# Kernel optimization log

Measured on AMD Instinct MI355X. Metric: run time of the kernel, lower is better.

The kernel has to match this reference:

```python
import jax, jax.numpy as jnp
import numpy as np

DIM = 2048
NUM_HEADS = 8
HEAD_DIM = DIM // NUM_HEADS  # 256; forward requires seq_len == HEAD_DIM
B = 64
N = HEAD_DIM  # q @ k (untransposed) only works when N == head_dim


def setup_inputs() -> dict:
    key = jax.random.key(0)
    k1, k2, k3, k4 = jax.random.split(key, 4)
    x = jax.random.normal(k1, (B, N, DIM), dtype=jnp.float32)
    # torch Linear stores weight as [out_features, in_features]
    w_qkv = jax.random.normal(k2, (3 * DIM, DIM), dtype=jnp.float32) * 0.02
    w_proj = jax.random.normal(k3, (DIM, DIM), dtype=jnp.float32) * 0.02
    b_proj = jax.random.normal(k4, (DIM,), dtype=jnp.float32) * 0.02
    return {"x": x, "w_qkv": w_qkv, "w_proj": w_proj, "b_proj": b_proj}


def reference(x, w_qkv, w_proj, b_proj):
    Bb, Nn, C = x.shape
    H, D = NUM_HEADS, C // NUM_HEADS
    # qkv projection (no bias), split into q,k,v of shape [B,H,N,D]
    qkv = (x @ w_qkv.T).reshape(Bb, Nn, 3, H, D).transpose(2, 0, 3, 1, 4)
    q, k, v = qkv[0], qkv[1], qkv[2]
    # NON-standard: q @ k with k NOT transposed -> contracts q's feature dim
    # against k's token dim (valid because D == N). attn: [B,H,N,N]
    attn = jnp.matmul(q, k)
    # transpose last two dims, then softmax over the new last axis
    attn = jnp.swapaxes(attn, -2, -1)
    attn = jax.nn.softmax(attn, axis=-1)
    out = jnp.matmul(attn, v)              # [B,H,N,D]
    out = out.swapaxes(1, 2).reshape(Bb, Nn, C)
    return out @ w_proj.T + b_proj
```

## Files before the change

### kernel.cpp

```cpp
#include <hip/hip_runtime.h>
#include <hip/hip_bf16.h>

typedef unsigned short u16;
typedef __attribute__((ext_vector_type(4))) float f32x4;
typedef __attribute__((ext_vector_type(8))) short short8;
typedef __attribute__((ext_vector_type(8))) u16 us8;


__device__ __forceinline__ u16 f2bf(float f) {
  union { float f; unsigned u; } v; v.f = f;
  unsigned r = v.u + 0x7fffu + ((v.u >> 16) & 1u);
  return (u16)(r >> 16);
}
__device__ __forceinline__ float bf2f(u16 h) {
  union { unsigned u; float f; } v; v.u = ((unsigned)h) << 16; return v.f;
}

__global__ void beacon_kernel(float* __restrict__ out, float val, int n) {
  int stride = gridDim.x * blockDim.x;
  for (int i = blockIdx.x * blockDim.x + threadIdx.x; i < n; i += stride)
    out[i] = val;
}

__global__ void split_kernel(const float* __restrict__ in, u16* __restrict__ hi,
                             u16* __restrict__ lo, int n4) {
  int stride = gridDim.x * blockDim.x;
  for (int i = blockIdx.x * blockDim.x + threadIdx.x; i < n4; i += stride) {
    f32x4 v = ((const f32x4*)in)[i];
    ushort4 h;
    h.x = f2bf(v[0]); h.y = f2bf(v[1]); h.z = f2bf(v[2]); h.w = f2bf(v[3]);
    ((ushort4*)hi)[i] = h;
    if (lo) {
      ushort4 l;
      l.x = f2bf(v[0] - bf2f(h.x)); l.y = f2bf(v[1] - bf2f(h.y));
      l.z = f2bf(v[2] - bf2f(h.z)); l.w = f2bf(v[3] - bf2f(h.w));
      ((ushort4*)lo)[i] = l;
    }
  }
}

#define LGKM0 do { asm volatile("s_waitcnt lgkmcnt(0)" ::: "memory"); \
                   __builtin_amdgcn_sched_barrier(0); } while (0)
#define VMDRAIN do { asm volatile("s_waitcnt vmcnt(0)" ::: "memory"); } while (0)
#define BAR __builtin_amdgcn_s_barrier()

template<int EPI>
__global__ __launch_bounds__(512, 2)
void gemm256(const u16* __restrict__ A0, const u16* __restrict__ A1,
             const u16* __restrict__ B0, const u16* __restrict__ B1,
             int ldA, int ldB, int ntiles, int segShift, int gridMx,
             u16* __restrict__ qh, u16* __restrict__ ql,
             u16* __restrict__ kh, u16* __restrict__ kl,
             u16* __restrict__ vv,
             float* __restrict__ fout, const float* __restrict__ bias) {
  extern __shared__ __align__(16) u16 lds[];

  const int tid = threadIdx.x;
  const int w = tid >> 6, lane = tid & 63;
  const int wr = w >> 2, wcn = w & 3;
  const int l15 = lane & 15, g = lane >> 4;
  const int rsw = l15 & 7;
  const int scol = (((tid & 7) ^ ((tid >> 3) & 7)) << 3);

  int bid = blockIdx.x, cpx = gridDim.x >> 3;
  int swz = (bid & 7) * cpx + (bid >> 3);
  int m0 = (swz % gridMx) << 8;
  int n0 = (swz / gridMx) << 8;

  const u16* As[2] = {A0, A1};
  const u16* Bs[2] = {B0, B1};
  const int kmask = (1 << segShift) - 1;

  f32x4 acc[8][4] = {};
  short8 af[8], bA[4], bB[4];

  auto stageA = [&](int db, const u16* Ab, int k0) {
    #pragma unroll
    for (int s = 0; s < 4; ++s) {
      const u16* src = Ab + (size_t)(m0 + s * 64 + (tid >> 3)) * ldA + k0 + scol;
      u16* dst = lds + db * 32768 + s * 4096 + tid * 8;
      __builtin_amdgcn_global_load_lds(
          (const __attribute__((address_space(1))) unsigned*)src,
          (__attribute__((address_space(3))) unsigned*)dst, 16, 0, 0);
    }
  };
  auto stageB = [&](int db, const u16* Bb, int k0) {
    #pragma unroll
    for (int s = 0; s < 4; ++s) {
      const u16* src = Bb + (size_t)(n0 + s * 64 + (tid >> 3)) * ldB + k0 + scol;
      u16* dst = lds + db * 32768 + 16384 + s * 4096 + tid * 8;
      __builtin_amdgcn_global_load_lds(
          (const __attribute__((address_space(1))) unsigned*)src,
          (__attribute__((address_space(3))) unsigned*)dst, 16, 0, 0);
    }
  };
  auto readA = [&](int db, int MH) {
    #pragma unroll
    for (int f = 0; f < 4; ++f) {
      int row = wr * 128 + MH * 64 + f * 16 + l15;
      #pragma unroll
      for (int kk = 0; kk < 2; ++kk) {
        int sl = (kk * 4 + g) ^ rsw;
        af[f * 2 + kk] = *(const short8*)(lds + db * 32768 + row * 64 + sl * 8);
      }
    }
  };
  auto readB = [&](short8* bf, int db, int NH) {
    #pragma unroll
    for (int f = 0; f < 2; ++f) {
      int row = wcn * 64 + NH * 32 + f * 16 + l15;
      #pragma unroll
      for (int kk = 0; kk < 2; ++kk) {
        int sl = (kk * 4 + g) ^ rsw;
        bf[f * 2 + kk] = *(const short8*)(lds + db * 32768 + 16384 + row * 64 + sl * 8);
      }
    }
  };

#define MMA_QUAD(MH, NH, BF)                                                   \
  __builtin_amdgcn_s_setprio(1);                                               \
  _Pragma("unroll") for (int f = 0; f < 4; ++f)                                \
    _Pragma("unroll") for (int j = 0; j < 2; ++j)                              \
      _Pragma("unroll") for (int kk = 0; kk < 2; ++kk)                         \
        acc[(MH) * 4 + f][(NH) * 2 + j] =                                      \
            __builtin_amdgcn_mfma_f32_16x16x32_bf16(                           \
                af[f * 2 + kk], BF[j * 2 + kk],                                \
                acc[(MH) * 4 + f][(NH) * 2 + j], 0, 0, 0);                     \
  __builtin_amdgcn_s_setprio(0)

  const int T = ntiles;
  stageA(0, As[0], 0);
  stageB(0, Bs[0], 0);
  VMDRAIN;
  BAR;
  __builtin_amdgcn_sched_barrier(0);

  for (int t = 0; t < T - 1; ++t) {
    int cur = t & 1, nxt = cur ^ 1;
    int t1 = t + 1;
    const u16* An = As[t1 >> segShift];
    const u16* Bn = Bs[t1 >> segShift];
    int kn = (t1 & kmask) << 6;
    readA(cur, 0);
    readB(bA, cur, 0);
    stageA(nxt, An, kn);
    BAR; LGKM0;
    MMA_QUAD(0, 0, bA);
    BAR; __builtin_amdgcn_sched_barrier(0);
    readB(bB, cur, 1);
    stageB(nxt, Bn, kn);
    BAR; LGKM0;
    MMA_QUAD(0, 1, bB);
    BAR; __builtin_amdgcn_sched_barrier(0);
    readA(cur, 1);
    BAR; LGKM0;
    MMA_QUAD(1, 1, bB);
    BAR; __builtin_amdgcn_sched_barrier(0);
    MMA_QUAD(1, 0, bA);
    VMDRAIN;
    BAR; __builtin_amdgcn_sched_barrier(0);
  }
  {
    int cur = (T - 1) & 1;
    readA(cur, 0);
    readB(bA, cur, 0);
    LGKM0;
    MMA_QUAD(0, 0, bA);
    readB(bB, cur, 1);
    LGKM0;
    MMA_QUAD(0, 1, bB);
    readA(cur, 1);
    LGKM0;
    MMA_QUAD(1, 1, bB);
    MMA_QUAD(1, 0, bA);
  }
#undef MMA_QUAD

  #pragma unroll
  for (int i = 0; i < 8; ++i)
    #pragma unroll
    for (int j = 0; j < 4; ++j)
      #pragma unroll
      for (int rr = 0; rr < 4; ++rr) {
        int gm = m0 + wr * 128 + i * 16 + g * 4 + rr;
        int gn = n0 + wcn * 64 + j * 16 + l15;
        float val = acc[i][j][rr];
        if constexpr (EPI == 0) {
          int b = gm >> 8, tok = gm & 255;
          int sel = gn >> 11, head = (gn >> 8) & 7, col = gn & 255;
          size_t addr = (((size_t)b * 8 + head) * 256 + tok) * 256 + col;
          u16 h = f2bf(val), lo = f2bf(val - bf2f(h));
          if (sel == 0) { qh[addr] = h; ql[addr] = lo; }
          else          { kh[addr] = h; kl[addr] = lo; }
        } else if constexpr (EPI == 1) {
          int b = gm >> 8, tok = gm & 255;
          int head = (gn >> 8) & 7, col = gn & 255;
          size_t addr = (((size_t)b * 8 + head) * 256 + tok) * 256 + col;
          vv[addr] = f2bf(val);
        } else {
          fout[(size_t)gm * 2048 + gn] = val + bias[gn];
        }
      }
}

template<int EPI, int SWZ>
__global__ __launch_bounds__(256)
void gemm_nt(const u16* __restrict__ A0, const u16* __restrict__ A1, const u16* __restrict__ A2,
             const u16* __restrict__ B0, const u16* __restrict__ B1, const u16* __restrict__ B2,
             float* __restrict__ sout, u16* __restrict__ aout,
             int ksteps, int segShift, int plane_base) {
  __shared__ __align__(16) u16 lds[8192];
  u16* sA = lds;
  u16* sB = lds + 4096;

  const int tid = threadIdx.x;
  const int wave = tid >> 6, lane = tid & 63;
  const int wr = wave >> 1, wc = wave & 1;
  const int l15 = lane & 15, l16 = lane >> 4;
  const int sxor = (l15 >> 1) & 3;

  size_t zoffA = 0, zoffB = 0;
  if constexpr (EPI == 2) {
    size_t gz = (size_t)(plane_base + blockIdx.z) * 65536;
    zoffA = gz; zoffB = gz;
  }
  if constexpr (EPI == 3) {
    zoffA = (size_t)blockIdx.z * 65536;
    zoffB = (size_t)(plane_base + blockIdx.z) * 65536;
  }
  const u16* As[3] = {A0 + zoffA, A1 + zoffA, A2 + zoffA};
  const u16* Bs[3] = {B0 + zoffB, B1 + zoffB, B2 + zoffB};

  const int m0 = blockIdx.x << 7;
  const int n0 = blockIdx.y << 7;
  const int kmask = (1 << segShift) - 1;

  f32x4 acc[4][4] = {};

  auto stage = [&](const u16* gp, int ld, u16* slot, int row0, int k0) {
    int scol = ((lane & 3) ^ ((lane >> 3) & 3)) * 8;
    #pragma unroll
    for (int c = 0; c < 2; ++c) {
      int chunk = wave + c * 4;
      int r = chunk * 16 + (lane >> 2);
      const u16* src = gp + (size_t)(row0 + r) * ld + (k0 + scol);
      __builtin_amdgcn_global_load_lds(
          (const __attribute__((address_space(1))) unsigned*)src,
          (__attribute__((address_space(3))) unsigned*)(slot + chunk * 512), 16, 0, 0);
    }
  };

  for (int ks = 0; ks < ksteps; ++ks) {
    int seg = ks >> segShift;
    int k0 = (ks & kmask) * 32;
    stage(As[seg], 256, sA, m0, k0);
    stage(Bs[seg], 256, sB, n0, k0);
    __syncthreads();

    short8 a[4], b[4];
    #pragma unroll
    for (int i = 0; i < 4; ++i) {
      int ra = (wr * 64 + i * 16 + l15) * 4 + (l16 ^ sxor);
      int rb = (wc * 64 + i * 16 + l15) * 4 + (l16 ^ sxor);
      a[i] = ((const short8*)sA)[ra];
      b[i] = ((const short8*)sB)[rb];
    }
    #pragma unroll
    for (int i = 0; i < 4; ++i)
      #pragma unroll
      for (int j = 0; j < 4; ++j)
        acc[i][j] = __builtin_amdgcn_mfma_f32_16x16x32_bf16(a[i], b[j], acc[i][j], 0, 0, 0);
    __syncthreads();
  }

  #pragma unroll
  for (int i = 0; i < 4; ++i)
    #pragma unroll
    for (int j = 0; j < 4; ++j)
      #pragma unroll
      for (int r = 0; r < 4; ++r) {
        int gm = m0 + wr * 64 + i * 16 + l16 * 4 + r;
        int gn = n0 + wc * 64 + j * 16 + l15;
        float val = acc[i][j][r];
        if constexpr (EPI == 2) {
          sout[(size_t)blockIdx.z * 65536 + (size_t)gm * 256 + gn] = val;
        } else {
          int gp = plane_base + blockIdx.z;
          size_t row = (size_t)(gp >> 3) * 256 + gm;
          size_t col = (size_t)(gp & 7) * 256 + gn;
          aout[row * 2048 + col] = f2bf(val);
        }
      }
}

__global__ void transpose_inplace(u16* __restrict__ kh, u16* __restrict__ kl,
                                  u16* __restrict__ v) {
  __shared__ u16 ta[64][66], tb[64][66];
  u16* base = (blockIdx.z == 0) ? kh : (blockIdx.z == 1) ? kl : v;
  u16* pl = base + (size_t)blockIdx.y * 65536;
  const int RA[10] = {0,1,2,3, 0,0,0,1,1,2};
  const int CA[10] = {0,1,2,3, 1,2,3,2,3,3};
  int p = blockIdx.x;
  int R = RA[p], C = CA[p];
  bool diag = (R == C);
  int tid = threadIdx.x;
  int r = tid >> 2, c0 = (tid & 3) * 16;

  const us8* sa = (const us8*)(pl + (size_t)(R * 64 + r) * 256 + C * 64 + c0);
  us8 a0 = sa[0], a1 = sa[1];
  #pragma unroll
  for (int s = 0; s < 8; ++s) { ta[r][c0 + s] = a0[s]; ta[r][c0 + 8 + s] = a1[s]; }
  if (!diag) {
    const us8* sb = (const us8*)(pl + (size_t)(C * 64 + r) * 256 + R * 64 + c0);
    us8 b0 = sb[0], b1 = sb[1];
    #pragma unroll
    for (int s = 0; s < 8; ++s) { tb[r][c0 + s] = b0[s]; tb[r][c0 + 8 + s] = b1[s]; }
  }
  __syncthreads();
  us8 o0, o1;
  #pragma unroll
  for (int s = 0; s < 8; ++s) { o0[s] = ta[c0 + s][r]; o1[s] = ta[c0 + 8 + s][r]; }
  us8* da = (us8*)(pl + (size_t)(C * 64 + r) * 256 + R * 64 + c0);
  da[0] = o0; da[1] = o1;
  if (!diag) {
    us8 p0, p1;
    #pragma unroll
    for (int s = 0; s < 8; ++s) { p0[s] = tb[c0 + s][r]; p1[s] = tb[c0 + 8 + s][r]; }
    us8* db = (us8*)(pl + (size_t)(R * 64 + r) * 256 + C * 64 + c0);
    db[0] = p0; db[1] = p1;
  }
}

__global__ void softmax_kernel(const float* __restrict__ S, u16* __restrict__ P) {
  int row = blockIdx.x * 4 + (threadIdx.x >> 6);
  int lane = threadIdx.x & 63;
  f32x4 v = ((const f32x4*)(S + (size_t)row * 256))[lane];
  float mx = fmaxf(fmaxf(v[0], v[1]), fmaxf(v[2], v[3]));
  #pragma unroll
  for (int o = 32; o > 0; o >>= 1) mx = fmaxf(mx, __shfl_xor(mx, o));
  float e0 = __expf(v[0] - mx), e1 = __expf(v[1] - mx);
  float e2 = __expf(v[2] - mx), e3 = __expf(v[3] - mx);
  float sum = e0 + e1 + e2 + e3;
  #pragma unroll
  for (int o = 32; o > 0; o >>= 1) sum += __shfl_xor(sum, o);
  float inv = 1.0f / sum;
  ushort4 p;
  p.x = f2bf(e0 * inv); p.y = f2bf(e1 * inv); p.z = f2bf(e2 * inv); p.w = f2bf(e3 * inv);
  ((ushort4*)(P + (size_t)row * 256))[lane] = p;
}

extern "C" void kernel_launch(void* const* d_in, const int* in_sizes, int n_in,
                              void* d_out, int out_size, void* d_ws, size_t ws_size,
                              hipStream_t stream) {
  const float* x  = (const float*)d_in[0];
  const float* wq = (const float*)d_in[1];
  const float* wp = (const float*)d_in[2];
  const float* bp = (const float*)d_in[3];
  float* out = (float*)d_out;
  char* ws = (char*)d_ws;

  const size_t MB = 1ull << 20;
  const size_t NEED = 432 * MB;
  if (ws_size < NEED) {
    beacon_kernel<<<2048, 256, 0, stream>>>(out, (float)(ws_size >> 20), 16384 * 2048);
    return;
  }

  u16* q_hi = (u16*)(ws);
  u16* q_lo = (u16*)(ws + 64 * MB);
  u16* k_hi = (u16*)(ws + 128 * MB);
  u16* k_lo = (u16*)(ws + 192 * MB);
  u16* vbuf = (u16*)(ws + 256 * MB);
  u16* x_hi = (u16*)(ws + 320 * MB);
  u16* w_hi = (u16*)(ws + 384 * MB);
  u16* w_lo = (u16*)(ws + 408 * MB);
  float* S  = (float*)(ws + 320 * MB);
  u16* Pm   = (u16*)(ws + 352 * MB);
  u16* attn = (u16*)(ws + 368 * MB);
  u16* wpb  = (u16*)(ws + 320 * MB);

  split_kernel<<<8192, 256, 0, stream>>>(x,  x_hi, nullptr, 16384 * 2048 / 4);
  split_kernel<<<4096, 256, 0, stream>>>(wq, w_hi, w_lo, 6144 * 2048 / 4);

  gemm256<0><<<1024, 512, 131072, stream>>>(
      x_hi, x_hi, w_hi, w_lo, 2048, 2048, 64, 5, 64,
      q_hi, q_lo, k_hi, k_lo, nullptr, nullptr, nullptr);
  const u16* wv = w_hi + (size_t)4096 * 2048;
  gemm256<1><<<512, 512, 131072, stream>>>(
      x_hi, x_hi, wv, wv, 2048, 2048, 32, 5, 64,
      nullptr, nullptr, nullptr, nullptr, vbuf, nullptr, nullptr);

  transpose_inplace<<<dim3(10, 512, 3), 256, 0, stream>>>(k_hi, k_lo, vbuf);

  for (int gp = 0; gp < 4; ++gp) {
    int pb = gp * 128;
    gemm_nt<2, 0><<<dim3(2, 2, 128), 256, 0, stream>>>(
        k_hi, k_hi, k_lo, q_hi, q_lo, q_hi,
        S, nullptr, 24, 3, pb);
    softmax_kernel<<<8192, 256, 0, stream>>>(S, Pm);
    gemm_nt<3, 0><<<dim3(2, 2, 128), 256, 0, stream>>>(
        Pm, Pm, Pm, vbuf, vbuf, vbuf,
        nullptr, attn, 8, 3, pb);
  }

  split_kernel<<<2048, 256, 0, stream>>>(wp, wpb, nullptr, 2048 * 2048 / 4);
  gemm256<2><<<512, 512, 131072, stream>>>(
      attn, attn, wpb, wpb, 2048, 2048, 32, 5, 64,
      nullptr, nullptr, nullptr, nullptr, nullptr, out, bp);
}
```

Baseline: 1.116 ms.

## Fuse score GEMM with softmax and batch all heads in single launches

Replaces the per-group score GEMM, fp32 S buffer, and separate softmax kernel with one attn_fused kernel. Each block computes full 256-wide rows of scores in registers and applies softmax in the epilogue, writing bf16 probabilities directly. The PV GEMM now runs over all 512 planes in one launch instead of four. This removes the fp32 score round-trip through memory and several launches, at the cost of higher register pressure (a 2x16 accumulator tile per wave), a larger LDS B tile, and scattered 2-byte stores for P.

New measurement: 1.093 ms. -2.0%, faster.

```diff
diff --git a/kernel.cpp b/kernel.cpp
--- a/kernel.cpp
+++ b/kernel.cpp
@@ -39,9 +39,9 @@
   }
 }
 
-#define LGKM0 do { asm volatile("s_waitcnt lgkmcnt(0)" ::: "memory"); \
-                   __builtin_amdgcn_sched_barrier(0); } while (0)
-#define VMDRAIN do { asm volatile("s_waitcnt vmcnt(0)" ::: "memory"); } while (0)
+#define SCHED0 __builtin_amdgcn_sched_barrier(0)
+#define LGKM0 do { asm volatile("s_waitcnt lgkmcnt(0)" ::: "memory"); SCHED0; } while (0)
+#define VM0 do { asm volatile("s_waitcnt vmcnt(0)" ::: "memory"); } while (0)
 #define BAR __builtin_amdgcn_s_barrier()
 
 template<int EPI>
@@ -131,9 +131,8 @@
   const int T = ntiles;
   stageA(0, As[0], 0);
   stageB(0, Bs[0], 0);
-  VMDRAIN;
-  BAR;
-  __builtin_amdgcn_sched_barrier(0);
+  VM0;
+  BAR; SCHED0;
 
   for (int t = 0; t < T - 1; ++t) {
     int cur = t & 1, nxt = cur ^ 1;
@@ -146,19 +145,19 @@
     stageA(nxt, An, kn);
     BAR; LGKM0;
     MMA_QUAD(0, 0, bA);
-    BAR; __builtin_amdgcn_sched_barrier(0);
+    BAR; SCHED0;
     readB(bB, cur, 1);
     stageB(nxt, Bn, kn);
     BAR; LGKM0;
     MMA_QUAD(0, 1, bB);
-    BAR; __builtin_amdgcn_sched_barrier(0);
+    BAR; SCHED0;
     readA(cur, 1);
     BAR; LGKM0;
     MMA_QUAD(1, 1, bB);
-    BAR; __builtin_amdgcn_sched_barrier(0);
+    BAR; SCHED0;
     MMA_QUAD(1, 0, bA);
-    VMDRAIN;
-    BAR; __builtin_amdgcn_sched_barrier(0);
+    VM0;
+    BAR; SCHED0;
   }
   {
     int cur = (T - 1) & 1;
@@ -203,12 +202,104 @@
       }
 }
 
-template<int EPI, int SWZ>
 __global__ __launch_bounds__(256)
-void gemm_nt(const u16* __restrict__ A0, const u16* __restrict__ A1, const u16* __restrict__ A2,
-             const u16* __restrict__ B0, const u16* __restrict__ B1, const u16* __restrict__ B2,
-             float* __restrict__ sout, u16* __restrict__ aout,
-             int ksteps, int segShift, int plane_base) {
+void attn_fused(const u16* __restrict__ kh, const u16* __restrict__ kl,
+                const u16* __restrict__ qh, const u16* __restrict__ ql,
+                u16* __restrict__ P) {
+  __shared__ __align__(16) u16 sA[4096];
+  __shared__ __align__(16) u16 sB[8192];
+  const int tid = threadIdx.x;
+  const int wave = tid >> 6, lane = tid & 63;
+  const int l15 = lane & 15, l16 = lane >> 4;
+  const int sxor = (l15 >> 1) & 3;
+  const int scol = ((lane & 3) ^ ((lane >> 3) & 3)) * 8;
+  const int m0 = blockIdx.x << 7;
+  const size_t zo = (size_t)blockIdx.y * 65536;
+  const u16* As[3] = {kh + zo, kh + zo, kl + zo};
+  const u16* Bs[3] = {qh + zo, ql + zo, qh + zo};
+
+  f32x4 acc[2][16] = {};
+
+  for (int ks = 0; ks < 24; ++ks) {
+    int seg = ks >> 3, k0 = (ks & 7) * 32;
+    {
+      const u16* gp = As[seg];
+      #pragma unroll
+      for (int c = 0; c < 2; ++c) {
+        int chunk = wave + c * 4;
+        int r = chunk * 16 + (lane >> 2);
+        const u16* src = gp + (size_t)(m0 + r) * 256 + k0 + scol;
+        __builtin_amdgcn_global_load_lds(
+            (const __attribute__((address_space(1))) unsigned*)src,
+            (__attribute__((address_space(3))) unsigned*)(sA + chunk * 512), 16, 0, 0);
+      }
+    }
+    {
+      const u16* gp = Bs[seg];
+      #pragma unroll
+      for (int c = 0; c < 4; ++c) {
+        int chunk = wave + c * 4;
+        int r = chunk * 16 + (lane >> 2);
+        const u16* src = gp + (size_t)r * 256 + k0 + scol;
+        __builtin_amdgcn_global_load_lds(
+            (const __attribute__((address_space(1))) unsigned*)src,
+            (__attribute__((address_space(3))) unsigned*)(sB + chunk * 512), 16, 0, 0);
+      }
+    }
+    __syncthreads();
+
+    short8 a[2];
+    #pragma unroll
+    for (int i = 0; i < 2; ++i) {
+      int ra = (wave * 32 + i * 16 + l15) * 4 + (l16 ^ sxor);
+      a[i] = ((const short8*)sA)[ra];
+    }
+    #pragma unroll
+    for (int h = 0; h < 2; ++h) {
+      short8 b[8];
+      #pragma unroll
+      for (int c = 0; c < 8; ++c) {
+        int rb = ((h * 8 + c) * 16 + l15) * 4 + (l16 ^ sxor);
+        b[c] = ((const short8*)sB)[rb];
+      }
+      #pragma unroll
+      for (int i = 0; i < 2; ++i)
+        #pragma unroll
+        for (int c = 0; c < 8; ++c)
+          acc[i][h * 8 + c] = __builtin_amdgcn_mfma_f32_16x16x32_bf16(
+              a[i], b[c], acc[i][h * 8 + c], 0, 0, 0);
+    }
+    __syncthreads();
+  }
+
+  u16* Pp = P + zo;
+  #pragma unroll
+  for (int i = 0; i < 2; ++i)
+    #pragma unroll
+    for (int rr = 0; rr < 4; ++rr) {
+      float m = acc[i][0][rr];
+      #pragma unroll
+      for (int c = 1; c < 16; ++c) m = fmaxf(m, acc[i][c][rr]);
+      #pragma unroll
+      for (int sh = 1; sh < 16; sh <<= 1) m = fmaxf(m, __shfl_xor(m, sh));
+      float e[16];
+      float s = 0.f;
+      #pragma unroll
+      for (int c = 0; c < 16; ++c) { e[c] = __expf(acc[i][c][rr] - m); s += e[c]; }
+      #pragma unroll
+      for (int sh = 1; sh < 16; sh <<= 1) s += __shfl_xor(s, sh);
+      float inv = 1.0f / s;
+      int row = m0 + wave * 32 + i * 16 + l16 * 4 + rr;
+      #pragma unroll
+      for (int c = 0; c < 16; ++c)
+        Pp[(size_t)row * 256 + c * 16 + l15] = f2bf(e[c] * inv);
+    }
+}
+
+template<int EPI>
+__global__ __launch_bounds__(256)
+void gemm_nt(const u16* __restrict__ A0, const u16* __restrict__ B0,
+             u16* __restrict__ aout, int ksteps) {
   __shared__ __align__(16) u16 lds[8192];
   u16* sA = lds;
   u16* sB = lds + 4096;
@@ -219,31 +310,22 @@
   const int l15 = lane & 15, l16 = lane >> 4;
   const int sxor = (l15 >> 1) & 3;
 
-  size_t zoffA = 0, zoffB = 0;
-  if constexpr (EPI == 2) {
-    size_t gz = (size_t)(plane_base + blockIdx.z) * 65536;
-    zoffA = gz; zoffB = gz;
-  }
-  if constexpr (EPI == 3) {
-    zoffA = (size_t)blockIdx.z * 65536;
-    zoffB = (size_t)(plane_base + blockIdx.z) * 65536;
-  }
-  const u16* As[3] = {A0 + zoffA, A1 + zoffA, A2 + zoffA};
-  const u16* Bs[3] = {B0 + zoffB, B1 + zoffB, B2 + zoffB};
+  size_t zoff = (size_t)blockIdx.z * 65536;
+  const u16* Ab = A0 + zoff;
+  const u16* Bb = B0 + zoff;
 
   const int m0 = blockIdx.x << 7;
   const int n0 = blockIdx.y << 7;
-  const int kmask = (1 << segShift) - 1;
 
   f32x4 acc[4][4] = {};
 
-  auto stage = [&](const u16* gp, int ld, u16* slot, int row0, int k0) {
+  auto stage = [&](const u16* gp, u16* slot, int row0, int k0) {
     int scol = ((lane & 3) ^ ((lane >> 3) & 3)) * 8;
     #pragma unroll
     for (int c = 0; c < 2; ++c) {
       int chunk = wave + c * 4;
       int r = chunk * 16 + (lane >> 2);
-      const u16* src = gp + (size_t)(row0 + r) * ld + (k0 + scol);
+      const u16* src = gp + (size_t)(row0 + r) * 256 + (k0 + scol);
       __builtin_amdgcn_global_load_lds(
           (const __attribute__((address_space(1))) unsigned*)src,
           (__attribute__((address_space(3))) unsigned*)(slot + chunk * 512), 16, 0, 0);
@@ -251,10 +333,9 @@
   };
 
   for (int ks = 0; ks < ksteps; ++ks) {
-    int seg = ks >> segShift;
-    int k0 = (ks & kmask) * 32;
-    stage(As[seg], 256, sA, m0, k0);
-    stage(Bs[seg], 256, sB, n0, k0);
+    int k0 = ks * 32;
+    stage(Ab, sA, m0, k0);
+    stage(Bb, sB, n0, k0);
     __syncthreads();
 
     short8 a[4], b[4];
@@ -281,15 +362,10 @@
       for (int r = 0; r < 4; ++r) {
         int gm = m0 + wr * 64 + i * 16 + l16 * 4 + r;
         int gn = n0 + wc * 64 + j * 16 + l15;
-        float val = acc[i][j][r];
-        if constexpr (EPI == 2) {
-          sout[(size_t)blockIdx.z * 65536 + (size_t)gm * 256 + gn] = val;
-        } else {
-          int gp = plane_base + blockIdx.z;
-          size_t row = (size_t)(gp >> 3) * 256 + gm;
-          size_t col = (size_t)(gp & 7) * 256 + gn;
-          aout[row * 2048 + col] = f2bf(val);
-        }
+        int gp = blockIdx.z;
+        size_t row = (size_t)(gp >> 3) * 256 + gm;
+        size_t col = (size_t)(gp & 7) * 256 + gn;
+        aout[row * 2048 + col] = f2bf(acc[i][j][r]);
       }
 }
 
@@ -331,24 +407,6 @@
   }
 }
 
-__global__ void softmax_kernel(const float* __restrict__ S, u16* __restrict__ P) {
-  int row = blockIdx.x * 4 + (threadIdx.x >> 6);
-  int lane = threadIdx.x & 63;
-  f32x4 v = ((const f32x4*)(S + (size_t)row * 256))[lane];
-  float mx = fmaxf(fmaxf(v[0], v[1]), fmaxf(v[2], v[3]));
-  #pragma unroll
-  for (int o = 32; o > 0; o >>= 1) mx = fmaxf(mx, __shfl_xor(mx, o));
-  float e0 = __expf(v[0] - mx), e1 = __expf(v[1] - mx);
-  float e2 = __expf(v[2] - mx), e3 = __expf(v[3] - mx);
-  float sum = e0 + e1 + e2 + e3;
-  #pragma unroll
-  for (int o = 32; o > 0; o >>= 1) sum += __shfl_xor(sum, o);
-  float inv = 1.0f / sum;
-  ushort4 p;
-  p.x = f2bf(e0 * inv); p.y = f2bf(e1 * inv); p.z = f2bf(e2 * inv); p.w = f2bf(e3 * inv);
-  ((ushort4*)(P + (size_t)row * 256))[lane] = p;
-}
-
 extern "C" void kernel_launch(void* const* d_in, const int* in_sizes, int n_in,
                               void* d_out, int out_size, void* d_ws, size_t ws_size,
                               hipStream_t stream) {
@@ -374,10 +432,9 @@
   u16* x_hi = (u16*)(ws + 320 * MB);
   u16* w_hi = (u16*)(ws + 384 * MB);
   u16* w_lo = (u16*)(ws + 408 * MB);
-  float* S  = (float*)(ws + 320 * MB);
-  u16* Pm   = (u16*)(ws + 352 * MB);
-  u16* attn = (u16*)(ws + 368 * MB);
-  u16* wpb  = (u16*)(ws + 320 * MB);
+  u16* Pm   = (u16*)(ws + 320 * MB);
+  u16* attn = (u16*)(ws + 128 * MB);
+  u16* wpb  = (u16*)(ws + 384 * MB);
 
   split_kernel<<<8192, 256, 0, stream>>>(x,  x_hi, nullptr, 16384 * 2048 / 4);
   split_kernel<<<4096, 256, 0, stream>>>(wq, w_hi, w_lo, 6144 * 2048 / 4);
@@ -392,16 +449,9 @@
 
   transpose_inplace<<<dim3(10, 512, 3), 256, 0, stream>>>(k_hi, k_lo, vbuf);
 
-  for (int gp = 0; gp < 4; ++gp) {
-    int pb = gp * 128;
-    gemm_nt<2, 0><<<dim3(2, 2, 128), 256, 0, stream>>>(
-        k_hi, k_hi, k_lo, q_hi, q_lo, q_hi,
-        S, nullptr, 24, 3, pb);
-    softmax_kernel<<<8192, 256, 0, stream>>>(S, Pm);
-    gemm_nt<3, 0><<<dim3(2, 2, 128), 256, 0, stream>>>(
-        Pm, Pm, Pm, vbuf, vbuf, vbuf,
-        nullptr, attn, 8, 3, pb);
-  }
+  attn_fused<<<dim3(2, 512), 256, 0, stream>>>(k_hi, k_lo, q_hi, q_lo, Pm);
+
+  gemm_nt<3><<<dim3(2, 2, 512), 256, 0, stream>>>(Pm, vbuf, attn, 8);
 
   split_kernel<<<2048, 256, 0, stream>>>(wp, wpb, nullptr, 2048 * 2048 / 4);
   gemm256<2><<<512, 512, 131072, stream>>>(
```
